# Performance work log

Hardware: AMD Instinct MI355X
Metric: run time of the kernel (lower is better)

Reference implementation:

```python
import jax, jax.numpy as jnp
import numpy as np

B, N, DIM = 8, 1024, 1024
HEADS, DIM_HEAD = 16, 64
INNER = HEADS * DIM_HEAD  # 1024


def setup_inputs() -> dict:
    key = jax.random.key(0)
    k1, k2, k3 = jax.random.split(key, 3)
    x = jax.random.normal(k1, (B, N, DIM), dtype=jnp.float32)
    # Dense kernels (Glorot-ish scale for numerical sanity)
    w_qkv = jax.random.normal(k2, (DIM, 3 * INNER), dtype=jnp.float32) * (DIM ** -0.5)
    w_out = jax.random.normal(k3, (INNER, DIM), dtype=jnp.float32) * (INNER ** -0.5)
    b_out = jnp.zeros((DIM,), dtype=jnp.float32)
    return {"x": x, "w_qkv": w_qkv, "w_out": w_out, "b_out": b_out}


def reference(x, w_qkv, w_out, b_out):
    scale = DIM_HEAD ** -0.5
    qkv = x @ w_qkv                                   # [B, N, 3*INNER]
    q, k, v = jnp.split(qkv, 3, axis=-1)              # each [B, N, INNER]

    def to_heads(t):
        # [B, N, H*Dh] -> [B, H, N, Dh]
        return t.reshape(B, N, HEADS, DIM_HEAD).transpose(0, 2, 1, 3)

    q, k, v = to_heads(q), to_heads(k), to_heads(v)
    dots = jnp.einsum("bhid,bhjd->bhij", q, k) * scale   # [B, H, N, N]
    attn = jax.nn.softmax(dots, axis=-1)
    out = jnp.einsum("bhij,bhjd->bhid", attn, v)          # [B, H, N, Dh]
    out = out.transpose(0, 2, 1, 3).reshape(B, N, INNER)  # merge heads
    return out @ w_out + b_out                            # project_out (dropout inactive at inference)
```

## Files before the change

### kernel.cpp

```cpp
#include <hip/hip_runtime.h>
#include <hip/hip_bf16.h>
#include <math.h>

typedef __bf16 bf16_t;
typedef __bf16 bf16x4 __attribute__((ext_vector_type(4)));
typedef __bf16 bf16x8 __attribute__((ext_vector_type(8)));
typedef float f32x4 __attribute__((ext_vector_type(4)));

#define LOG2E 1.44269504088896340736f

#define GL2LDS(g, l)                                                     \
  __builtin_amdgcn_global_load_lds(                                      \
      (const __attribute__((address_space(1))) unsigned int*)(g),        \
      (__attribute__((address_space(3))) unsigned int*)(l), 16, 0, 0)

#define BAR() asm volatile("s_barrier" ::: "memory")
#define VMCNT(n) asm volatile("s_waitcnt vmcnt(" #n ")" ::: "memory")
#define LGKM0()                                         \
  do {                                                  \
    asm volatile("s_waitcnt lgkmcnt(0)" ::: "memory");  \
    __builtin_amdgcn_sched_barrier(0);                  \
  } while (0)

__global__ __launch_bounds__(256) void convert_f32_bf16(const float* __restrict__ in,
                                                        bf16_t* __restrict__ out) {
  const size_t idx = (size_t)(blockIdx.x * 256 + threadIdx.x) * 8;
  f32x4 a = *(const f32x4*)&in[idx];
  f32x4 b = *(const f32x4*)&in[idx + 4];
  bf16x8 v;
#pragma unroll
  for (int i = 0; i < 4; i++) { v[i] = (bf16_t)a[i]; v[i + 4] = (bf16_t)b[i]; }
  *(bf16x8*)&out[idx] = v;
}

__global__ __launch_bounds__(256) void transpose_f32_bf16(const float* __restrict__ in,
                                                          bf16_t* __restrict__ out,
                                                          int R, int C) {
  __shared__ bf16_t t[64][65];
  const int c0 = blockIdx.x * 64, r0 = blockIdx.y * 64;
  const int tx = threadIdx.x, ty = threadIdx.y;
#pragma unroll
  for (int i = 0; i < 16; i++) {
    int r = ty + i * 4;
    t[r][tx] = (bf16_t)in[(size_t)(r0 + r) * C + c0 + tx];
  }
  __syncthreads();
#pragma unroll
  for (int i = 0; i < 16; i++) {
    int r = ty + i * 4;
    out[(size_t)(c0 + r) * R + r0 + tx] = t[tx][r];
  }
}

template <int MODE>
__global__ __launch_bounds__(256, 4) void gemmT(const bf16_t* __restrict__ A,
                                                const bf16_t* __restrict__ Bt,
                                                bf16_t* __restrict__ Qb,
                                                bf16_t* __restrict__ Kb,
                                                bf16_t* __restrict__ Vtb,
                                                const float* __restrict__ bias,
                                                float* __restrict__ Out) {
  constexpr int K = 1024;
  constexpr int NT = K / 32;
  __shared__ __align__(16) bf16_t As[3][128 * 32];
  __shared__ __align__(16) bf16_t Bs[3][128 * 32];
  const int gx = gridDim.x;
  const int lin = blockIdx.y * gx + blockIdx.x;
  const int per = (gx * gridDim.y) >> 3;
  const int swz = (lin & 7) * per + (lin >> 3);
  const int m0 = (swz / gx) * 128, n0 = (swz % gx) * 128;
  const int tid = threadIdx.x;
  const int w = tid >> 6, l = tid & 63;
  const int lr = l & 15, lq = l >> 4;
  const int wm = w >> 1, wn = w & 1;

  const int rs = tid >> 2, ps = tid & 3;
  const int cs = (ps ^ ((rs >> 1) & 3)) * 8;
  const size_t gA0 = (size_t)(m0 + rs) * K + cs;
  const size_t gA1 = (size_t)(m0 + 64 + rs) * K + cs;
  const size_t gB0 = (size_t)(n0 + rs) * K + cs;
  const size_t gB1 = (size_t)(n0 + 64 + rs) * K + cs;
  const int ldsu0 = (w * 64) * 8;
  const int ldsu1 = (256 + w * 64) * 8;

#define STG(bf_, kt_)                                   \
  do {                                                  \
    const size_t kk_ = (size_t)(kt_) * 32;              \
    GL2LDS(&A[gA0 + kk_], &As[bf_][ldsu0]);             \
    GL2LDS(&A[gA1 + kk_], &As[bf_][ldsu1]);             \
    GL2LDS(&Bt[gB0 + kk_], &Bs[bf_][ldsu0]);            \
    GL2LDS(&Bt[gB1 + kk_], &Bs[bf_][ldsu1]);            \
  } while (0)

  int aoff[4], boff[4];
#pragma unroll
  for (int mf = 0; mf < 4; mf++) {
    const int row = wm * 64 + mf * 16 + lr;
    aoff[mf] = row * 32 + ((lq ^ ((row >> 1) & 3)) << 3);
  }
#pragma unroll
  for (int nf = 0; nf < 4; nf++) {
    const int row = wn * 64 + nf * 16 + lr;
    boff[nf] = row * 32 + ((lq ^ ((row >> 1) & 3)) << 3);
  }

  f32x4 acc[4][4] = {};

  STG(0, 0);
  STG(1, 1);
  VMCNT(4);
  BAR();

  for (int t = 0; t < NT; ++t) {
    const int bufR = t % 3;
    if (t + 2 < NT) STG((t + 2) % 3, t + 2);
    bf16x8 af[4], bv[4];
#pragma unroll
    for (int mf = 0; mf < 4; mf++)
      af[mf] = *(const bf16x8*)&As[bufR][aoff[mf]];
#pragma unroll
    for (int nf = 0; nf < 4; nf++)
      bv[nf] = *(const bf16x8*)&Bs[bufR][boff[nf]];
    LGKM0();
    __builtin_amdgcn_s_setprio(1);
#pragma unroll
    for (int mf = 0; mf < 4; mf++)
#pragma unroll
      for (int nf = 0; nf < 4; nf++)
        acc[mf][nf] = __builtin_amdgcn_mfma_f32_16x16x32_bf16(af[mf], bv[nf],
                                                              acc[mf][nf], 0, 0, 0);
    __builtin_amdgcn_s_setprio(0);
    if (t == NT - 2) { VMCNT(0); } else if (t < NT - 2) { VMCNT(4); }
    BAR();
  }

#pragma unroll
  for (int mf = 0; mf < 4; mf++)
#pragma unroll
    for (int nf = 0; nf < 4; nf++)
#pragma unroll
      for (int i = 0; i < 4; i++) {
        const int m = m0 + wm * 64 + mf * 16 + lq * 4 + i;
        const int c = n0 + wn * 64 + nf * 16 + lr;
        const float v = acc[mf][nf][i];
        if (MODE == 1) {
          Out[(size_t)m * 1024 + c] = v + bias[c];
        } else {
          const int b = m >> 10, n = m & 1023;
          const int which = c >> 10, cc = c & 1023;
          const int hh = cc >> 6, d = cc & 63;
          const size_t qk = ((size_t)((b * 16 + hh) * 1024 + n)) * 64 + d;
          if (which == 0)
            Qb[qk] = (bf16_t)(v * (0.125f * LOG2E));
          else if (which == 1)
            Kb[qk] = (bf16_t)v;
          else
            Vtb[((size_t)((b * 16 + hh) * 64 + d)) * 1024 + n] = (bf16_t)v;
        }
      }
}

#define KVS 68
#define PS  72
__global__ __launch_bounds__(256) void attn128(const bf16_t* __restrict__ Qb,
                                               const bf16_t* __restrict__ Kb,
                                               const bf16_t* __restrict__ Vtb,
                                               bf16_t* __restrict__ Ob) {
  __shared__ __align__(16) bf16_t Ks[2][64 * KVS];
  __shared__ __align__(16) bf16_t Vs[2][64 * KVS];
  __shared__ __align__(16) bf16_t Pl[4 * 32 * PS];
  const int bid = blockIdx.x;
  const int qt = bid >> 7, b = (bid >> 4) & 7, h = bid & 15;
  const bf16_t* Qh = Qb + (size_t)((b * 16 + h) * 1024) * 64;
  const bf16_t* Kh = Kb + (size_t)((b * 16 + h) * 1024) * 64;
  const bf16_t* Vh = Vtb + (size_t)((b * 16 + h) * 64) * 1024;
  const int tid = threadIdx.x, w = tid >> 6, l = tid & 63;
  const int lr = l & 15, lq = l >> 4;
  const int q0 = qt * 128 + w * 32;
  const int swz = (lr >> 1) & 3;

  bf16x8 onesA;
#pragma unroll
  for (int i = 0; i < 8; i++) onesA[i] = (bf16_t)1.0f;

  const int sr = tid >> 3, sc = tid & 7;

  bf16x8 qf[2][2];
#pragma unroll
  for (int mf = 0; mf < 2; mf++)
#pragma unroll
    for (int ks = 0; ks < 2; ks++)
      qf[mf][ks] = *(const bf16x8*)&Qh[(size_t)(q0 + mf * 16 + lr) * 64 + ks * 32 + lq * 8];

  {
    bf16x8 k0 = *(const bf16x8*)&Kh[(size_t)sr * 64 + sc * 8];
    bf16x8 k1 = *(const bf16x8*)&Kh[(size_t)(sr + 32) * 64 + sc * 8];
    bf16x8 v0 = *(const bf16x8*)&Vh[(size_t)sr * 1024 + sc * 8];
    bf16x8 v1 = *(const bf16x8*)&Vh[(size_t)(sr + 32) * 1024 + sc * 8];
    *(bf16x8*)&Ks[0][sr * KVS + sc * 8] = k0;
    *(bf16x8*)&Ks[0][(sr + 32) * KVS + sc * 8] = k1;
    *(bf16x8*)&Vs[0][sr * KVS + sc * 8] = v0;
    *(bf16x8*)&Vs[0][(sr + 32) * KVS + sc * 8] = v1;
  }
  __syncthreads();

  f32x4 o[4][2] = {};
  f32x4 o5[2] = {};
  bf16_t* pw = &Pl[w * 32 * PS];

  for (int it = 0; it < 16; ++it) {
    const int buf = it & 1;
    bf16x8 nk0, nk1, nv0, nv1;
    if (it < 15) {
      const int jn = (it + 1) * 64;
      nk0 = *(const bf16x8*)&Kh[(size_t)(jn + sr) * 64 + sc * 8];
      nk1 = *(const bf16x8*)&Kh[(size_t)(jn + sr + 32) * 64 + sc * 8];
      nv0 = *(const bf16x8*)&Vh[(size_t)sr * 1024 + jn + sc * 8];
      nv1 = *(const bf16x8*)&Vh[(size_t)(sr + 32) * 1024 + jn + sc * 8];
    }
    f32x4 s[4][2] = {};
#pragma unroll
    for (int ks = 0; ks < 2; ks++)
#pragma unroll
      for (int nf = 0; nf < 4; nf++) {
        bf16x8 kf = *(const bf16x8*)&Ks[buf][(nf * 16 + lr) * KVS + ks * 32 + lq * 8];
#pragma unroll
        for (int mf = 0; mf < 2; mf++)
          s[nf][mf] = __builtin_amdgcn_mfma_f32_16x16x32_bf16(kf, qf[mf][ks], s[nf][mf], 0, 0, 0);
      }
#pragma unroll
    for (int mf = 0; mf < 2; mf++)
#pragma unroll
      for (int nf = 0; nf < 4; nf++) {
        bf16x4 pk;
#pragma unroll
        for (int i = 0; i < 4; i++) pk[i] = (bf16_t)exp2f(s[nf][mf][i]);
        *(bf16x4*)&pw[(mf * 16 + lr) * PS + (((nf * 2 + (lq >> 1)) ^ swz) << 3) +
                      (lq & 1) * 4] = pk;
      }
#pragma unroll
    for (int ks = 0; ks < 2; ks++) {
      bf16x8 pf[2];
#pragma unroll
      for (int mf = 0; mf < 2; mf++)
        pf[mf] = *(const bf16x8*)&pw[(mf * 16 + lr) * PS + ((ks * 4 + (lq ^ swz)) << 3)];
#pragma unroll
      for (int df = 0; df < 4; df++) {
        bf16x8 vf = *(const bf16x8*)&Vs[buf][(df * 16 + lr) * KVS + ks * 32 + lq * 8];
#pragma unroll
        for (int mf = 0; mf < 2; mf++)
          o[df][mf] = __builtin_amdgcn_mfma_f32_16x16x32_bf16(vf, pf[mf], o[df][mf], 0, 0, 0);
      }
#pragma unroll
      for (int mf = 0; mf < 2; mf++)
        o5[mf] = __builtin_amdgcn_mfma_f32_16x16x32_bf16(onesA, pf[mf], o5[mf], 0, 0, 0);
    }
    if (it < 15) {
      *(bf16x8*)&Ks[buf ^ 1][sr * KVS + sc * 8] = nk0;
      *(bf16x8*)&Ks[buf ^ 1][(sr + 32) * KVS + sc * 8] = nk1;
      *(bf16x8*)&Vs[buf ^ 1][sr * KVS + sc * 8] = nv0;
      *(bf16x8*)&Vs[buf ^ 1][(sr + 32) * KVS + sc * 8] = nv1;
    }
    __syncthreads();
  }
#pragma unroll
  for (int mf = 0; mf < 2; mf++) {
    const float inv = 1.0f / o5[mf][0];
    const int grow = b * 1024 + q0 + mf * 16 + lr;
#pragma unroll
    for (int df = 0; df < 4; df++) {
      bf16x4 ov;
#pragma unroll
      for (int i = 0; i < 4; i++) ov[i] = (bf16_t)(o[df][mf][i] * inv);
      *(bf16x4*)&Ob[(size_t)grow * 1024 + h * 64 + df * 16 + lq * 4] = ov;
    }
  }
}

extern "C" void kernel_launch(void* const* d_in, const int* in_sizes, int n_in,
                              void* d_out, int out_size, void* d_ws, size_t ws_size,
                              hipStream_t stream) {
  const float* x     = (const float*)d_in[0];
  const float* w_qkv = (const float*)d_in[1];
  const float* w_out = (const float*)d_in[2];
  const float* b_out = (const float*)d_in[3];
  float* out = (float*)d_out;

  bf16_t* ws = (bf16_t*)d_ws;
  const size_t SZ = (size_t)8 * 1024 * 1024;
  bf16_t* Qb  = ws;
  bf16_t* Kb  = Qb + SZ;
  bf16_t* Vtb = Kb + SZ;
  bf16_t* Ob  = Vtb + SZ;
  bf16_t* Wqt = Ob + SZ;
  bf16_t* Wot = Wqt + (size_t)3072 * 1024;
  bf16_t* Xb  = Ob;

  hipLaunchKernelGGL(convert_f32_bf16, dim3(4096), dim3(256), 0, stream, x, Xb);
  hipLaunchKernelGGL(transpose_f32_bf16, dim3(48, 16), dim3(64, 4), 0, stream,
                     w_qkv, Wqt, 1024, 3072);
  hipLaunchKernelGGL(transpose_f32_bf16, dim3(16, 16), dim3(64, 4), 0, stream,
                     w_out, Wot, 1024, 1024);
  hipLaunchKernelGGL((gemmT<0>), dim3(24, 64), dim3(256), 0, stream,
                     Xb, Wqt, Qb, Kb, Vtb, (const float*)nullptr, (float*)nullptr);
  hipLaunchKernelGGL(attn128, dim3(1024), dim3(256), 0, stream, Qb, Kb, Vtb, Ob);
  hipLaunchKernelGGL((gemmT<1>), dim3(8, 64), dim3(256), 0, stream,
                     Ob, Wot, (bf16_t*)nullptr, (bf16_t*)nullptr, (bf16_t*)nullptr,
                     b_out, out);
}
```

Before: 283.6 us.

## Stage K/V tiles via direct global-to-LDS loads with XOR swizzle

Replaces the register-staged K/V double buffering in the attention kernel with global_load_lds DMA into unpadded, XOR-swizzled LDS tiles. The swizzle on 16-byte chunks is meant to avoid bank conflicts without padding. It also raises wave priority around the MFMA sections. This removes the VGPRs that held the prefetched tiles and the LDS store instructions, at the cost of an explicit vmcnt wait before each barrier.

Measured after the change: 276.0 us. 1.03x faster.

```diff
diff --git a/kernel.cpp b/kernel.cpp
--- a/kernel.cpp
+++ b/kernel.cpp
@@ -160,14 +160,13 @@
       }
 }
 
-#define KVS 68
 #define PS  72
 __global__ __launch_bounds__(256) void attn128(const bf16_t* __restrict__ Qb,
                                                const bf16_t* __restrict__ Kb,
                                                const bf16_t* __restrict__ Vtb,
                                                bf16_t* __restrict__ Ob) {
-  __shared__ __align__(16) bf16_t Ks[2][64 * KVS];
-  __shared__ __align__(16) bf16_t Vs[2][64 * KVS];
+  __shared__ __align__(16) bf16_t Ks[2][64 * 64];
+  __shared__ __align__(16) bf16_t Vs[2][64 * 64];
   __shared__ __align__(16) bf16_t Pl[4 * 32 * PS];
   const int bid = blockIdx.x;
   const int qt = bid >> 7, b = (bid >> 4) & 7, h = bid & 15;
@@ -178,12 +177,28 @@
   const int lr = l & 15, lq = l >> 4;
   const int q0 = qt * 128 + w * 32;
   const int swz = (lr >> 1) & 3;
+  const int g7 = (lr >> 1) & 7;
+  const int kc0 = (lq ^ g7) * 8;
+  const int kc1 = ((4 + lq) ^ g7) * 8;
 
   bf16x8 onesA;
 #pragma unroll
   for (int i = 0; i < 8; i++) onesA[i] = (bf16_t)1.0f;
 
-  const int sr = tid >> 3, sc = tid & 7;
+  const int r0 = tid >> 3, r1 = r0 + 32, p0 = tid & 7;
+  const int ck0 = (p0 ^ ((r0 >> 1) & 7)) * 8;
+  const int ck1 = (p0 ^ ((r1 >> 1) & 7)) * 8;
+  const int ldsS0 = (w * 64) * 8;
+  const int ldsS1 = (256 + w * 64) * 8;
+
+#define STGKV(bf_, j_)                                                  \
+  do {                                                                  \
+    const size_t jb = (size_t)(j_) * 64;                                \
+    GL2LDS(&Kh[(jb + r0) * 64 + ck0], &Ks[bf_][ldsS0]);                 \
+    GL2LDS(&Kh[(jb + r1) * 64 + ck1], &Ks[bf_][ldsS1]);                 \
+    GL2LDS(&Vh[(size_t)r0 * 1024 + jb + ck0], &Vs[bf_][ldsS0]);         \
+    GL2LDS(&Vh[(size_t)r1 * 1024 + jb + ck1], &Vs[bf_][ldsS1]);         \
+  } while (0)
 
   bf16x8 qf[2][2];
 #pragma unroll
@@ -192,17 +207,9 @@
     for (int ks = 0; ks < 2; ks++)
       qf[mf][ks] = *(const bf16x8*)&Qh[(size_t)(q0 + mf * 16 + lr) * 64 + ks * 32 + lq * 8];
 
-  {
-    bf16x8 k0 = *(const bf16x8*)&Kh[(size_t)sr * 64 + sc * 8];
-    bf16x8 k1 = *(const bf16x8*)&Kh[(size_t)(sr + 32) * 64 + sc * 8];
-    bf16x8 v0 = *(const bf16x8*)&Vh[(size_t)sr * 1024 + sc * 8];
-    bf16x8 v1 = *(const bf16x8*)&Vh[(size_t)(sr + 32) * 1024 + sc * 8];
-    *(bf16x8*)&Ks[0][sr * KVS + sc * 8] = k0;
-    *(bf16x8*)&Ks[0][(sr + 32) * KVS + sc * 8] = k1;
-    *(bf16x8*)&Vs[0][sr * KVS + sc * 8] = v0;
-    *(bf16x8*)&Vs[0][(sr + 32) * KVS + sc * 8] = v1;
-  }
-  __syncthreads();
+  STGKV(0, 0);
+  VMCNT(0);
+  BAR();
 
   f32x4 o[4][2] = {};
   f32x4 o5[2] = {};
@@ -210,24 +217,19 @@
 
   for (int it = 0; it < 16; ++it) {
     const int buf = it & 1;
-    bf16x8 nk0, nk1, nv0, nv1;
-    if (it < 15) {
-      const int jn = (it + 1) * 64;
-      nk0 = *(const bf16x8*)&Kh[(size_t)(jn + sr) * 64 + sc * 8];
-      nk1 = *(const bf16x8*)&Kh[(size_t)(jn + sr + 32) * 64 + sc * 8];
-      nv0 = *(const bf16x8*)&Vh[(size_t)sr * 1024 + jn + sc * 8];
-      nv1 = *(const bf16x8*)&Vh[(size_t)(sr + 32) * 1024 + jn + sc * 8];
-    }
+    if (it < 15) STGKV(buf ^ 1, it + 1);
     f32x4 s[4][2] = {};
+    __builtin_amdgcn_s_setprio(1);
 #pragma unroll
     for (int ks = 0; ks < 2; ks++)
 #pragma unroll
       for (int nf = 0; nf < 4; nf++) {
-        bf16x8 kf = *(const bf16x8*)&Ks[buf][(nf * 16 + lr) * KVS + ks * 32 + lq * 8];
+        bf16x8 kf = *(const bf16x8*)&Ks[buf][(nf * 16 + lr) * 64 + (ks ? kc1 : kc0)];
 #pragma unroll
         for (int mf = 0; mf < 2; mf++)
           s[nf][mf] = __builtin_amdgcn_mfma_f32_16x16x32_bf16(kf, qf[mf][ks], s[nf][mf], 0, 0, 0);
       }
+    __builtin_amdgcn_s_setprio(0);
 #pragma unroll
     for (int mf = 0; mf < 2; mf++)
 #pragma unroll
@@ -238,6 +240,7 @@
         *(bf16x4*)&pw[(mf * 16 + lr) * PS + (((nf * 2 + (lq >> 1)) ^ swz) << 3) +
                       (lq & 1) * 4] = pk;
       }
+    __builtin_amdgcn_s_setprio(1);
 #pragma unroll
     for (int ks = 0; ks < 2; ks++) {
       bf16x8 pf[2];
@@ -246,7 +249,7 @@
         pf[mf] = *(const bf16x8*)&pw[(mf * 16 + lr) * PS + ((ks * 4 + (lq ^ swz)) << 3)];
 #pragma unroll
       for (int df = 0; df < 4; df++) {
-        bf16x8 vf = *(const bf16x8*)&Vs[buf][(df * 16 + lr) * KVS + ks * 32 + lq * 8];
+        bf16x8 vf = *(const bf16x8*)&Vs[buf][(df * 16 + lr) * 64 + (ks ? kc1 : kc0)];
 #pragma unroll
         for (int mf = 0; mf < 2; mf++)
           o[df][mf] = __builtin_amdgcn_mfma_f32_16x16x32_bf16(vf, pf[mf], o[df][mf], 0, 0, 0);
@@ -255,13 +258,9 @@
       for (int mf = 0; mf < 2; mf++)
         o5[mf] = __builtin_amdgcn_mfma_f32_16x16x32_bf16(onesA, pf[mf], o5[mf], 0, 0, 0);
     }
-    if (it < 15) {
-      *(bf16x8*)&Ks[buf ^ 1][sr * KVS + sc * 8] = nk0;
-      *(bf16x8*)&Ks[buf ^ 1][(sr + 32) * KVS + sc * 8] = nk1;
-      *(bf16x8*)&Vs[buf ^ 1][sr * KVS + sc * 8] = nv0;
-      *(bf16x8*)&Vs[buf ^ 1][(sr + 32) * KVS + sc * 8] = nv1;
-    }
-    __syncthreads();
+    __builtin_amdgcn_s_setprio(0);
+    VMCNT(0);
+    BAR();
   }
 #pragma unroll
   for (int mf = 0; mf < 2; mf++) {
```
